# Optimization experiments

Hardware: AMD Instinct MI355X
Metric: run time of the kernel (lower is better)

## Reference

```python
import jax, jax.numpy as jnp
import numpy as np

# dims
B, S = 1, 32768          # batch, grid seqlen (32^3 latent grid)
NQ, NE = 32768, 262144   # mesh query nodes, grid->query edges
IN, EMB, HID, BOT, PREDH, OUT, NDIM = 192, 192, 192, 192, 192, 4, 3
MAX_WAVELENGTH = 10000.0


def sincos_embed(coords, dim, ndim):
    # ContinuousSincosEmbed: dim % ndim == 0 and (dim//ndim) even here -> no padding
    eff = dim // ndim                                     # 64 dims per coordinate
    omega = 1.0 / MAX_WAVELENGTH ** (jnp.arange(0, eff, 2, dtype=jnp.float32) / eff)  # [eff//2]
    out = coords[..., None] * omega                       # [N, ndim, eff//2]
    emb = jnp.concatenate([jnp.sin(out), jnp.cos(out)], axis=-1)  # [N, ndim, eff]
    return emb.reshape(coords.shape[0], ndim * eff)       # [N, dim]


def _linear_params(key, fan_in, fan_out):
    k1, k2 = jax.random.split(key)
    lim = 1.0 / np.sqrt(fan_in)
    w = jax.random.uniform(k1, (fan_in, fan_out), jnp.float32, -lim, lim)
    b = jax.random.uniform(k2, (fan_out,), jnp.float32, -lim, lim)
    return w, b


def setup_inputs() -> dict:
    key = jax.random.key(0)
    ks = jax.random.split(key, 10)
    x = jax.random.normal(ks[0], (B, S, IN), jnp.float32)
    query_pos = jax.random.uniform(ks[1], (NQ, NDIM), jnp.float32) * 100.0
    # edges sorted by query index (required by the CSR segment reduce in the original)
    qidx = jnp.sort(jax.random.randint(ks[2], (NE,), 0, NQ))
    gidx = jax.random.randint(ks[3], (NE,), 0, B * S)
    grid_to_query_edges = jnp.stack([qidx, gidx], axis=1).astype(jnp.int64)
    proj_w, proj_b = _linear_params(ks[4], IN, EMB)
    msg0_w, msg0_b = _linear_params(ks[5], 2 * EMB, 2 * HID)
    msg1_w, msg1_b = _linear_params(ks[6], 2 * HID, 2 * HID)
    msg2_w, msg2_b = _linear_params(ks[7], 2 * HID, BOT)
    pred0_w, pred0_b = _linear_params(ks[8], BOT, PREDH)
    pred1_w, pred1_b = _linear_params(ks[9], PREDH, OUT)
    return dict(x=x, query_pos=query_pos, grid_to_query_edges=grid_to_query_edges,
                proj_w=proj_w, proj_b=proj_b,
                msg0_w=msg0_w, msg0_b=msg0_b, msg1_w=msg1_w, msg1_b=msg1_b,
                msg2_w=msg2_w, msg2_b=msg2_b,
                pred0_w=pred0_w, pred0_b=pred0_b, pred1_w=pred1_w, pred1_b=pred1_b)


def reference(x, query_pos, grid_to_query_edges,
              proj_w, proj_b, msg0_w, msg0_b, msg1_w, msg1_b, msg2_w, msg2_b,
              pred0_w, pred0_b, pred1_w, pred1_b):
    gelu = lambda t: jax.nn.gelu(t, approximate=False)  # torch nn.GELU default (erf)
    # flatten grid tokens and project
    xf = x.reshape(-1, x.shape[-1]) @ proj_w + proj_b          # [B*S, EMB]
    qe = sincos_embed(query_pos, EMB, NDIM)                    # [NQ, EMB]
    qidx = grid_to_query_edges[:, 0]
    gidx = grid_to_query_edges[:, 1]
    # gather + concat per edge
    h = jnp.concatenate([xf[gidx], qe[qidx]], axis=1)          # [NE, 2*EMB]
    # message MLP
    h = gelu(h @ msg0_w + msg0_b)
    h = gelu(h @ msg1_w + msg1_b)
    h = h @ msg2_w + msg2_b                                    # [NE, BOT]
    # segment mean to query nodes (empty segments -> 0, matching segment_csr mean)
    nq = query_pos.shape[0]
    seg_sum = jax.ops.segment_sum(h, qidx, num_segments=nq)    # [NQ, BOT]
    cnt = jax.ops.segment_sum(jnp.ones((qidx.shape[0], 1), h.dtype), qidx, num_segments=nq)
    m = seg_sum / jnp.maximum(cnt, 1.0)
    # prediction head
    out = gelu(m @ pred0_w + pred0_b) @ pred1_w + pred1_b      # [NQ, OUT]
    return out
```

## Files before the change

### kernel.cpp

```cpp
#include <hip/hip_runtime.h>
#include <math.h>

#define N_Q    32768
#define N_E    262144

typedef _Float16 half8 __attribute__((ext_vector_type(8)));
typedef _Float16 half4v __attribute__((ext_vector_type(4)));
typedef float f32x4 __attribute__((ext_vector_type(4)));

__device__ __forceinline__ float gelu_f(float x) {
    float ax = fabsf(x);
    float z = ax * 0.7071067811865476f;
    float t = __builtin_amdgcn_rcpf(fmaf(0.3275911f, z, 1.0f));
    float poly = t * fmaf(t, fmaf(t, fmaf(t, fmaf(t, 1.061405429f, -1.453152027f),
                                          1.421413741f), -0.284496736f), 0.254829592f);
    float u = fmaf(-poly, __expf(-z * z), 1.0f);
    return fmaf(0.5f * ax, u, 0.5f * x);
}

__global__ __launch_bounds__(256) void embed_kernel(const float* __restrict__ qpos,
                                                    _Float16* __restrict__ qe) {
    int gid = blockIdx.x * 256 + threadIdx.x;
    int q = gid / 192, c = gid - q * 192;
    int d = c >> 6, j = c & 63;
    int i = j & 31;
    float omega = expf(-(float)i * (9.210340371976184f / 32.0f));
    float arg = qpos[q * 3 + d] * omega;
    qe[gid] = (_Float16)((j < 32) ? sinf(arg) : cosf(arg));
}

__global__ __launch_bounds__(256) void pack_w_kernel(const float* __restrict__ W,
                                                     _Float16* __restrict__ Wp,
                                                     int K, int N) {
    int u = blockIdx.x * 256 + threadIdx.x;
    if (u * 8 >= K * N) return;
    int l = u & 63, blk = u >> 6;
    int nks = K >> 5;
    int ntile = blk / nks, ks = blk - ntile * nks;
    int n = ntile * 16 + (l & 15);
    int k0 = ks * 32 + (l >> 4) * 8;
    half8 v;
    #pragma unroll
    for (int j = 0; j < 8; ++j) v[j] = (_Float16)W[(size_t)(k0 + j) * N + n];
    *(half8*)(Wp + (size_t)u * 8) = v;
}

#define PK 200

__global__ __launch_bounds__(256, 2) void proj_mfma_kernel(
    const float* __restrict__ x, const _Float16* __restrict__ Wp,
    const float* __restrict__ bias, _Float16* __restrict__ xf)
{
    __shared__ _Float16 hA[64 * PK];
    const int t = threadIdx.x;
    const int r0 = blockIdx.x * 64;
    const int lane = t & 63;
    const int w = t >> 6;
    const int ln = lane & 15, lq = lane >> 4;

    #pragma unroll
    for (int i = 0; i < 12; ++i) {
        int idx = t + 256 * i;
        int r = idx / 48, c4 = idx - r * 48;
        float4 v = ((const float4*)(x + (size_t)(r0 + r) * 192))[c4];
        half4v hv; hv[0] = (_Float16)v.x; hv[1] = (_Float16)v.y;
        hv[2] = (_Float16)v.z; hv[3] = (_Float16)v.w;
        *(half4v*)(hA + r * PK + c4 * 4) = hv;
    }
    __syncthreads();

    f32x4 acc[4][3];
    #pragma unroll
    for (int nt = 0; nt < 3; ++nt) {
        float bv = bias[w * 48 + nt * 16 + ln];
        #pragma unroll
        for (int mt = 0; mt < 4; ++mt) acc[mt][nt] = (f32x4){bv, bv, bv, bv};
    }
    #pragma unroll 2
    for (int ks = 0; ks < 6; ++ks) {
        half8 a[4], bf[3];
        #pragma unroll
        for (int mt = 0; mt < 4; ++mt)
            a[mt] = *(const half8*)(hA + (mt * 16 + ln) * PK + ks * 32 + lq * 8);
        #pragma unroll
        for (int nt = 0; nt < 3; ++nt)
            bf[nt] = *(const half8*)(Wp + (size_t)(((w * 3 + nt) * 6 + ks) * 512 + lane * 8));
        #pragma unroll
        for (int nt = 0; nt < 3; ++nt)
            #pragma unroll
            for (int mt = 0; mt < 4; ++mt)
                acc[mt][nt] = __builtin_amdgcn_mfma_f32_16x16x32_f16(a[mt], bf[nt], acc[mt][nt], 0, 0, 0);
    }
    #pragma unroll
    for (int mt = 0; mt < 4; ++mt)
        #pragma unroll
        for (int nt = 0; nt < 3; ++nt)
            #pragma unroll
            for (int r = 0; r < 4; ++r) {
                int m = mt * 16 + lq * 4 + r;
                int n = w * 48 + nt * 16 + ln;
                xf[(size_t)(r0 + m) * 192 + n] = (_Float16)acc[mt][nt][r];
            }
}

#define PADK 392

__global__ __launch_bounds__(512, 4) void edge_mlp_kernel(
    const _Float16* __restrict__ xf, const _Float16* __restrict__ qe,
    const int* __restrict__ edges,
    const _Float16* __restrict__ Wp0, const float* __restrict__ b0,
    const _Float16* __restrict__ Wp1, const float* __restrict__ b1,
    const _Float16* __restrict__ Wp2, const float* __restrict__ b2,
    float* __restrict__ seg, float* __restrict__ cnt)
{
    __shared__ _Float16 hA[64 * PADK];
    __shared__ int qi[64], gi[64];
    float* h2 = (float*)hA;

    const int t = threadIdx.x;
    const int e0 = blockIdx.x * 64;
    const int lane = t & 63;
    const int w = t >> 6;
    const int ln = lane & 15;
    const int lq = lane >> 4;

    if (t < 64) {
        qi[t] = edges[2 * (e0 + t)];
        gi[t] = edges[2 * (e0 + t) + 1];
    }
    __syncthreads();

    #pragma unroll
    for (int i = 0; i < 6; ++i) {
        int idx = t + 512 * i;
        int m = idx / 48, c = idx - m * 48;
        const half8* src = (c < 24) ? ((const half8*)(xf + (size_t)gi[m] * 192) + c)
                                    : ((const half8*)(qe + (size_t)qi[m] * 192) + (c - 24));
        *(half8*)(hA + m * PADK + c * 8) = *src;
    }
    __syncthreads();

    #pragma unroll 1
    for (int L = 0; L < 2; ++L) {
        const _Float16* __restrict__ Wp = L ? Wp1 : Wp0;
        const float* __restrict__ bias = L ? b1 : b0;

        f32x4 acc[4][3];
        #pragma unroll
        for (int nt = 0; nt < 3; ++nt) {
            float bv = bias[w * 48 + nt * 16 + ln];
            #pragma unroll
            for (int mt = 0; mt < 4; ++mt)
                acc[mt][nt] = (f32x4){bv, bv, bv, bv};
        }
        #pragma unroll 2
        for (int ks = 0; ks < 12; ++ks) {
            half8 a[4], bf[3];
            #pragma unroll
            for (int mt = 0; mt < 4; ++mt)
                a[mt] = *(const half8*)(hA + (mt * 16 + ln) * PADK + ks * 32 + lq * 8);
            #pragma unroll
            for (int nt = 0; nt < 3; ++nt)
                bf[nt] = *(const half8*)(Wp + (size_t)(((w * 3 + nt) * 12 + ks) * 512 + lane * 8));
            #pragma unroll
            for (int nt = 0; nt < 3; ++nt)
                #pragma unroll
                for (int mt = 0; mt < 4; ++mt)
                    acc[mt][nt] = __builtin_amdgcn_mfma_f32_16x16x32_f16(a[mt], bf[nt], acc[mt][nt], 0, 0, 0);
        }
        __syncthreads();
        #pragma unroll
        for (int mt = 0; mt < 4; ++mt)
            #pragma unroll
            for (int nt = 0; nt < 3; ++nt)
                #pragma unroll
                for (int r = 0; r < 4; ++r) {
                    int m = mt * 16 + lq * 4 + r;
                    int n = w * 48 + nt * 16 + ln;
                    hA[m * PADK + n] = (_Float16)gelu_f(acc[mt][nt][r]);
                }
        __syncthreads();
    }

    {
        const int n0 = (w & 3) * 48;
        const int mh = (w >> 2) * 2;
        f32x4 acc[2][3];
        #pragma unroll
        for (int nt = 0; nt < 3; ++nt) {
            float bv = b2[n0 + nt * 16 + ln];
            #pragma unroll
            for (int mt = 0; mt < 2; ++mt)
                acc[mt][nt] = (f32x4){bv, bv, bv, bv};
        }
        #pragma unroll 2
        for (int ks = 0; ks < 12; ++ks) {
            half8 a[2], bf[3];
            #pragma unroll
            for (int mt = 0; mt < 2; ++mt)
                a[mt] = *(const half8*)(hA + ((mh + mt) * 16 + ln) * PADK + ks * 32 + lq * 8);
            #pragma unroll
            for (int nt = 0; nt < 3; ++nt)
                bf[nt] = *(const half8*)(Wp2 + (size_t)((((w & 3) * 3 + nt) * 12 + ks) * 512 + lane * 8));
            #pragma unroll
            for (int nt = 0; nt < 3; ++nt)
                #pragma unroll
                for (int mt = 0; mt < 2; ++mt)
                    acc[mt][nt] = __builtin_amdgcn_mfma_f32_16x16x32_f16(a[mt], bf[nt], acc[mt][nt], 0, 0, 0);
        }
        __syncthreads();
        #pragma unroll
        for (int mt = 0; mt < 2; ++mt)
            #pragma unroll
            for (int nt = 0; nt < 3; ++nt)
                #pragma unroll
                for (int r = 0; r < 4; ++r) {
                    int m = (mh + mt) * 16 + lq * 4 + r;
                    int n = n0 + nt * 16 + ln;
                    h2[m * 192 + n] = acc[mt][nt][r];
                }
        __syncthreads();
    }

    if (t < 192) {
        float a = 0.0f;
        for (int m = 0; m < 64; ++m) {
            a += h2[m * 192 + t];
            if (m == 63 || qi[m + 1] != qi[m]) {
                atomicAdd(&seg[(size_t)qi[m] * 192 + t], a);
                a = 0.0f;
            }
        }
    } else if (t == 192) {
        float run = 1.0f;
        for (int m = 1; m < 64; ++m) {
            if (qi[m] != qi[m - 1]) { atomicAdd(&cnt[qi[m - 1]], run); run = 1.0f; }
            else run += 1.0f;
        }
        atomicAdd(&cnt[qi[63]], run);
    }
}

#define PSK 196

__global__ __launch_bounds__(256, 2) void head_kernel(
    const float* __restrict__ seg, const float* __restrict__ cnt,
    const _Float16* __restrict__ Wp0, const float* __restrict__ b0,
    const float* __restrict__ w1, const float* __restrict__ b1,
    float* __restrict__ out)
{
    __shared__ _Float16 hA[64 * PK];
    __shared__ float ps[64 * PSK];
    __shared__ float w1s[192 * 4];
    __shared__ float invc[64];
    const int t = threadIdx.x;
    const int r0 = blockIdx.x * 64;
    const int lane = t & 63;
    const int w = t >> 6;
    const int ln = lane & 15, lq = lane >> 4;

    if (t < 64) invc[t] = 1.0f / fmaxf(cnt[r0 + t], 1.0f);
    if (t < 192) ((float4*)w1s)[t] = ((const float4*)w1)[t];
    __syncthreads();

    #pragma unroll
    for (int i = 0; i < 12; ++i) {
        int idx = t + 256 * i;
        int r = idx / 48, c4 = idx - r * 48;
        float inv = invc[r];
        float4 v = ((const float4*)(seg + (size_t)(r0 + r) * 192))[c4];
        half4v hv; hv[0] = (_Float16)(v.x * inv); hv[1] = (_Float16)(v.y * inv);
        hv[2] = (_Float16)(v.z * inv); hv[3] = (_Float16)(v.w * inv);
        *(half4v*)(hA + r * PK + c4 * 4) = hv;
    }
    __syncthreads();

    f32x4 acc[4][3];
    #pragma unroll
    for (int nt = 0; nt < 3; ++nt) {
        float bv = b0[w * 48 + nt * 16 + ln];
        #pragma unroll
        for (int mt = 0; mt < 4; ++mt) acc[mt][nt] = (f32x4){bv, bv, bv, bv};
    }
    #pragma unroll 2
    for (int ks = 0; ks < 6; ++ks) {
        half8 a[4], bf[3];
        #pragma unroll
        for (int mt = 0; mt < 4; ++mt)
            a[mt] = *(const half8*)(hA + (mt * 16 + ln) * PK + ks * 32 + lq * 8);
        #pragma unroll
        for (int nt = 0; nt < 3; ++nt)
            bf[nt] = *(const half8*)(Wp0 + (size_t)(((w * 3 + nt) * 6 + ks) * 512 + lane * 8));
        #pragma unroll
        for (int nt = 0; nt < 3; ++nt)
            #pragma unroll
            for (int mt = 0; mt < 4; ++mt)
                acc[mt][nt] = __builtin_amdgcn_mfma_f32_16x16x32_f16(a[mt], bf[nt], acc[mt][nt], 0, 0, 0);
    }
    #pragma unroll
    for (int mt = 0; mt < 4; ++mt)
        #pragma unroll
        for (int nt = 0; nt < 3; ++nt)
            #pragma unroll
            for (int r = 0; r < 4; ++r) {
                int m = mt * 16 + lq * 4 + r;
                int n = w * 48 + nt * 16 + ln;
                ps[m * PSK + n] = gelu_f(acc[mt][nt][r]);
            }
    __syncthreads();

    {
        int r = t >> 2, oo = t & 3;
        float a = b1[oo];
        for (int k = 0; k < 192; ++k)
            a = fmaf(ps[r * PSK + k], w1s[k * 4 + oo], a);
        out[(size_t)(r0 + r) * 4 + oo] = a;
    }
}

extern "C" void kernel_launch(void* const* d_in, const int* in_sizes, int n_in,
                              void* d_out, int out_size, void* d_ws, size_t ws_size,
                              hipStream_t stream) {
    (void)in_sizes; (void)n_in; (void)out_size; (void)ws_size;
    const float* x       = (const float*)d_in[0];
    const float* qpos    = (const float*)d_in[1];
    const int*   edges   = (const int*)d_in[2];
    const float* proj_w  = (const float*)d_in[3];
    const float* proj_b  = (const float*)d_in[4];
    const float* msg0_w  = (const float*)d_in[5];
    const float* msg0_b  = (const float*)d_in[6];
    const float* msg1_w  = (const float*)d_in[7];
    const float* msg1_b  = (const float*)d_in[8];
    const float* msg2_w  = (const float*)d_in[9];
    const float* msg2_b  = (const float*)d_in[10];
    const float* pred0_w = (const float*)d_in[11];
    const float* pred0_b = (const float*)d_in[12];
    const float* pred1_w = (const float*)d_in[13];
    const float* pred1_b = (const float*)d_in[14];
    float* out = (float*)d_out;

    char* ws = (char*)d_ws;
    _Float16* xf  = (_Float16*)(ws);
    _Float16* qe  = (_Float16*)(ws + 12582912);
    float*    seg = (float*)(ws + 25165824);
    float*    cnt = (float*)(ws + 50331648);
    _Float16* Wp0 = (_Float16*)(ws + 50462720);
    _Float16* Wp1 = (_Float16*)(ws + 50757632);
    _Float16* Wp2 = (_Float16*)(ws + 51052544);
    _Float16* WpP = (_Float16*)(ws + 51200000);
    _Float16* WpH = (_Float16*)(ws + 51273728);

    hipMemsetAsync(seg, 0, 25165824 + 131072, stream);
    embed_kernel<<<24576, 256, 0, stream>>>(qpos, qe);
    pack_w_kernel<<<18, 256, 0, stream>>>(proj_w,  WpP, 192, 192);
    pack_w_kernel<<<72, 256, 0, stream>>>(msg0_w, Wp0, 384, 384);
    pack_w_kernel<<<72, 256, 0, stream>>>(msg1_w, Wp1, 384, 384);
    pack_w_kernel<<<36, 256, 0, stream>>>(msg2_w, Wp2, 384, 192);
    pack_w_kernel<<<18, 256, 0, stream>>>(pred0_w, WpH, 192, 192);
    proj_mfma_kernel<<<512, 256, 0, stream>>>(x, WpP, proj_b, xf);
    edge_mlp_kernel<<<4096, 512, 0, stream>>>(xf, qe, edges,
                                              Wp0, msg0_b, Wp1, msg1_b, Wp2, msg2_b,
                                              seg, cnt);
    head_kernel<<<512, 256, 0, stream>>>(seg, cnt, WpH, pred0_b,
                                         pred1_w, pred1_b, out);
}
```

Measured before the change: 406.1 us.

## Merge weight packing launches, cheapen GELU and sincos, split segment reduce

Replaces the five weight-packing launches with one kernel that dispatches on block index. The embedding kernel now computes sin and cos together with hardware sin/cos after range reduction, and GELU switches to a shorter 3-term erf polynomial with exp2. The edge MLP raises its occupancy hint from 4 to 6 and splits the final segment reduction across two halves of the threads. The lower-order erf approximation and hardware trig reduce accuracy, and the occupancy change may force register spills.

Result: faster. 372.4 us (-8.3%).

```diff
diff --git a/kernel.cpp b/kernel.cpp
--- a/kernel.cpp
+++ b/kernel.cpp
@@ -10,29 +10,33 @@
 
 __device__ __forceinline__ float gelu_f(float x) {
     float ax = fabsf(x);
-    float z = ax * 0.7071067811865476f;
-    float t = __builtin_amdgcn_rcpf(fmaf(0.3275911f, z, 1.0f));
-    float poly = t * fmaf(t, fmaf(t, fmaf(t, fmaf(t, 1.061405429f, -1.453152027f),
-                                          1.421413741f), -0.284496736f), 0.254829592f);
-    float u = fmaf(-poly, __expf(-z * z), 1.0f);
-    return fmaf(0.5f * ax, u, 0.5f * x);
+    float t = __builtin_amdgcn_rcpf(fmaf(0.33269070724668f, ax, 1.0f));
+    float poly = t * fmaf(t, fmaf(t, 0.7478556f, -0.0958798f), 0.3480242f);
+    float e = exp2f(-0.72134752044448f * ax * ax);
+    float u = fmaf(-poly, e, 1.0f);
+    return 0.5f * fmaf(ax, u, x);
 }
 
 __global__ __launch_bounds__(256) void embed_kernel(const float* __restrict__ qpos,
                                                     _Float16* __restrict__ qe) {
     int gid = blockIdx.x * 256 + threadIdx.x;
-    int q = gid / 192, c = gid - q * 192;
-    int d = c >> 6, j = c & 63;
-    int i = j & 31;
-    float omega = expf(-(float)i * (9.210340371976184f / 32.0f));
+    int q = gid / 96, r = gid - q * 96;
+    int d = r >> 5, i = r & 31;
+    float omega = exp2f(-(float)i * 0.41524101186092029f);
     float arg = qpos[q * 3 + d] * omega;
-    qe[gid] = (_Float16)((j < 32) ? sinf(arg) : cosf(arg));
-}
-
-__global__ __launch_bounds__(256) void pack_w_kernel(const float* __restrict__ W,
-                                                     _Float16* __restrict__ Wp,
-                                                     int K, int N) {
-    int u = blockIdx.x * 256 + threadIdx.x;
+    float rev = arg * 0.15915494309189535f;
+    rev = rev - floorf(rev);
+    float s = __builtin_amdgcn_sinf(rev);
+    float c = __builtin_amdgcn_cosf(rev);
+    int base = q * 192 + d * 64 + i;
+    qe[base] = (_Float16)s;
+    qe[base + 32] = (_Float16)c;
+}
+
+__device__ __forceinline__ void pack_one(const float* __restrict__ W,
+                                         _Float16* __restrict__ Wp,
+                                         int K, int N, int blk0, int tid) {
+    int u = blk0 * 256 + tid;
     if (u * 8 >= K * N) return;
     int l = u & 63, blk = u >> 6;
     int nks = K >> 5;
@@ -43,6 +47,20 @@
     #pragma unroll
     for (int j = 0; j < 8; ++j) v[j] = (_Float16)W[(size_t)(k0 + j) * N + n];
     *(half8*)(Wp + (size_t)u * 8) = v;
+}
+
+__global__ __launch_bounds__(256) void pack_all_kernel(
+    const float* __restrict__ pw,  _Float16* __restrict__ WpP,
+    const float* __restrict__ m0,  _Float16* __restrict__ Wp0,
+    const float* __restrict__ m1,  _Float16* __restrict__ Wp1,
+    const float* __restrict__ m2,  _Float16* __restrict__ Wp2,
+    const float* __restrict__ hw,  _Float16* __restrict__ WpH) {
+    int b = blockIdx.x, t = threadIdx.x;
+    if      (b < 18)  pack_one(pw, WpP, 192, 192, b,        t);
+    else if (b < 90)  pack_one(m0, Wp0, 384, 384, b - 18,   t);
+    else if (b < 162) pack_one(m1, Wp1, 384, 384, b - 90,   t);
+    else if (b < 198) pack_one(m2, Wp2, 384, 192, b - 162,  t);
+    else              pack_one(hw, WpH, 192, 192, b - 198,  t);
 }
 
 #define PK 200
@@ -105,7 +123,7 @@
 
 #define PADK 392
 
-__global__ __launch_bounds__(512, 4) void edge_mlp_kernel(
+__global__ __launch_bounds__(512, 6) void edge_mlp_kernel(
     const _Float16* __restrict__ xf, const _Float16* __restrict__ qe,
     const int* __restrict__ edges,
     const _Float16* __restrict__ Wp0, const float* __restrict__ b0,
@@ -222,22 +240,27 @@
         __syncthreads();
     }
 
-    if (t < 192) {
+    if (t < 384) {
+        int half = t >= 192;
+        int col = t - half * 192;
+        int mlo = half * 32, mhi = mlo + 32;
         float a = 0.0f;
-        for (int m = 0; m < 64; ++m) {
-            a += h2[m * 192 + t];
-            if (m == 63 || qi[m + 1] != qi[m]) {
-                atomicAdd(&seg[(size_t)qi[m] * 192 + t], a);
+        for (int m = mlo; m < mhi; ++m) {
+            a += h2[m * 192 + col];
+            if (m == mhi - 1 || qi[m + 1] != qi[m]) {
+                atomicAdd(&seg[(size_t)qi[m] * 192 + col], a);
                 a = 0.0f;
             }
         }
-    } else if (t == 192) {
+    } else if (t < 386) {
+        int half = t - 384;
+        int mlo = half * 32, mhi = mlo + 32;
         float run = 1.0f;
-        for (int m = 1; m < 64; ++m) {
+        for (int m = mlo + 1; m < mhi; ++m) {
             if (qi[m] != qi[m - 1]) { atomicAdd(&cnt[qi[m - 1]], run); run = 1.0f; }
             else run += 1.0f;
         }
-        atomicAdd(&cnt[qi[63]], run);
+        atomicAdd(&cnt[qi[mhi - 1]], run);
     }
 }
 
@@ -351,12 +374,10 @@
     _Float16* WpH = (_Float16*)(ws + 51273728);
 
     hipMemsetAsync(seg, 0, 25165824 + 131072, stream);
-    embed_kernel<<<24576, 256, 0, stream>>>(qpos, qe);
-    pack_w_kernel<<<18, 256, 0, stream>>>(proj_w,  WpP, 192, 192);
-    pack_w_kernel<<<72, 256, 0, stream>>>(msg0_w, Wp0, 384, 384);
-    pack_w_kernel<<<72, 256, 0, stream>>>(msg1_w, Wp1, 384, 384);
-    pack_w_kernel<<<36, 256, 0, stream>>>(msg2_w, Wp2, 384, 192);
-    pack_w_kernel<<<18, 256, 0, stream>>>(pred0_w, WpH, 192, 192);
+    embed_kernel<<<12288, 256, 0, stream>>>(qpos, qe);
+    pack_all_kernel<<<216, 256, 0, stream>>>(proj_w, WpP, msg0_w, Wp0,
+                                             msg1_w, Wp1, msg2_w, Wp2,
+                                             pred0_w, WpH);
     proj_mfma_kernel<<<512, 256, 0, stream>>>(x, WpP, proj_b, xf);
     edge_mlp_kernel<<<4096, 512, 0, stream>>>(xf, qe, edges,
                                               Wp0, msg0_b, Wp1, msg1_b, Wp2, msg2_b,
```
